# Optimization experiments

Hardware: AMD Instinct MI355X
Metric: run time of the kernel (lower is better)

Reference implementation:

```python
import jax, jax.numpy as jnp
import numpy as np

N_PTS = 500_000
NP_NODES = 258
L_DOMAIN = 10.0
TP = 1.0 - 1.0 / 150.0  # threshold_p
TM = 1.0 + 1.0 / 150.0  # threshold_m


def setup_inputs() -> dict:
    key = jax.random.key(0)
    k_x, _ = jax.random.split(key)
    x = jax.random.uniform(k_x, (N_PTS, 1), dtype=jnp.float32) * L_DOMAIN
    coordinates = jnp.linspace(0.0, L_DOMAIN, NP_NODES, dtype=jnp.float32)
    w_uu = jnp.ones((NP_NODES - 2,), dtype=jnp.float32)   # NodalValues_uu init
    w_dd = jnp.zeros((2,), dtype=jnp.float32)             # [u_0, u_L] = [0, 0]
    return {"x": x, "coordinates": coordinates, "w_uu": w_uu, "w_dd": w_dd}


def _hat(x, xm, xi, xp):
    # Piecewise-linear 'hat' basis: LinearBlock(left) + LinearBlock(right) + l2 bias (-1)
    left = jax.nn.relu(jax.nn.relu(xi - x) * (-1.0 / (xi - xm)) + 1.0)
    right = jax.nn.relu(jax.nn.relu(x - xi) * (-1.0 / (xp - xi)) + 1.0)
    return left + right - 1.0


def reference(x, coordinates, w_uu, w_dd):
    c = coordinates
    # Interior nodes i = 1 .. np-2 (vectorized over all shape functions)
    xm = c[:-2]          # x_{i-1}, shape [np-2]
    xi = c[1:-1]         # x_i
    xp = c[2:]           # x_{i+1}
    xi = jnp.maximum(jnp.minimum(xi, TP * xp), TM * xm)
    phi_uu = _hat(x, xm, xi, xp)          # [N, np-2] via broadcast of x [N,1]

    # Boundary shape functions (Shapefunction(-1) and Shapefunction(-2))
    xm0 = c[0] - c[-1] / 100.0
    xi0 = jnp.maximum(jnp.minimum(c[0], TP * c[1]), TM * xm0)
    xpL = c[-1] * (1.0 + 1.0 / 100.0)
    xiL = jnp.maximum(jnp.minimum(c[-1], TP * xpL), TM * c[-2])
    phi_0 = _hat(x, xm0, xi0, c[1])       # [N, 1]
    phi_L = _hat(x, c[-2], xiL, xpL)      # [N, 1]
    phi_dd = jnp.concatenate([phi_0, phi_L], axis=1)  # [N, 2]

    # InterpoLayer_uu + InterpoLayer_dd + SumLayer (weights all ones -> sum)
    u = phi_uu @ w_uu + phi_dd @ w_dd     # [N]
    return u[:, None]                     # [N, 1]
```

## Files before the change

kernel.cpp:

```cpp
#include <hip/hip_runtime.h>


#define TPf ((float)(1.0 - 1.0 / 150.0))
#define TMf ((float)(1.0 + 1.0 / 150.0))

__device__ __forceinline__ float hat_eval(float x, float xm, float xi, float xp) {
    float l = fmaxf(fmaxf(xi - x, 0.0f) * (-1.0f / (xi - xm)) + 1.0f, 0.0f);
    float r = fmaxf(fmaxf(x - xi, 0.0f) * (-1.0f / (xp - xi)) + 1.0f, 0.0f);
    return l + r - 1.0f;
}

__global__ __launch_bounds__(256) void MeshNN_29042568855825_kernel(
    const float* __restrict__ X,
    const float* __restrict__ C,
    const float* __restrict__ Wu,
    const float* __restrict__ Wd,
    float* __restrict__ Out,
    int n)
{
    __shared__ float sc[258];
    __shared__ float sw[256];
    __shared__ float swd[2];
    const int tid = threadIdx.x;
    for (int j = tid; j < 258; j += 256) sc[j] = C[j];
    sw[tid] = Wu[tid];
    if (tid < 2) swd[tid] = Wd[tid];
    __syncthreads();

    const float c0 = sc[0], c1 = sc[1], cNm2 = sc[256], cNm1 = sc[257];
    const float xm0 = c0 - cNm1 / 100.0f;
    const float xi0 = fmaxf(fminf(c0, TPf * c1), TMf * xm0);
    const float xpL = cNm1 * (float)(1.0 + 1.0 / 100.0);
    const float xiL = fmaxf(fminf(cNm1, TPf * xpL), TMf * cNm2);
    const float inv_h = 257.0f / (cNm1 - c0);
    const float wd0 = swd[0], wd1 = swd[1];

    const int g = blockIdx.x * 256 + tid;
    const int base = g * 4;
    if (base >= n) return;

    float xs[4];
    const bool full = (base + 3) < n;
    if (full) {
        float4 xv = ((const float4*)X)[g];
        xs[0] = xv.x; xs[1] = xv.y; xs[2] = xv.z; xs[3] = xv.w;
    } else {
        #pragma unroll
        for (int k = 0; k < 4; ++k) xs[k] = (base + k < n) ? X[base + k] : 0.0f;
    }

    float us[4];
    #pragma unroll
    for (int k = 0; k < 4; ++k) {
        const float x = xs[k];
        int i = (int)((x - c0) * inv_h);
        i = min(max(i, 0), 256);
        while (i > 0 && x < sc[i]) --i;
        while (i < 256 && x >= sc[i + 1]) ++i;

        float u = wd0 * hat_eval(x, xm0, xi0, c1)
                + wd1 * hat_eval(x, cNm2, xiL, xpL);

        if (i >= 1) {
            const float xm = sc[i - 1], xr = sc[i], xp = sc[i + 1];
            const float xic = fmaxf(fminf(xr, TPf * xp), TMf * xm);
            u += sw[i - 1] * hat_eval(x, xm, xic, xp);
        }
        if (i <= 255) {
            const float xm = sc[i], xr = sc[i + 1], xp = sc[i + 2];
            const float xic = fmaxf(fminf(xr, TPf * xp), TMf * xm);
            u += sw[i] * hat_eval(x, xm, xic, xp);
        }
        us[k] = u;
    }

    if (full) {
        ((float4*)Out)[g] = make_float4(us[0], us[1], us[2], us[3]);
    } else {
        #pragma unroll
        for (int k = 0; k < 4; ++k)
            if (base + k < n) Out[base + k] = us[k];
    }
}

extern "C" void kernel_launch(void* const* d_in, const int* in_sizes, int n_in,
                              void* d_out, int out_size, void* d_ws, size_t ws_size,
                              hipStream_t stream) {
    const float* x  = (const float*)d_in[0];
    const float* c  = (const float*)d_in[1];
    const float* wu = (const float*)d_in[2];
    const float* wd = (const float*)d_in[3];
    float* out = (float*)d_out;

    const int n = in_sizes[0];
    const int ngroups = (n + 3) / 4;
    const int blocks = (ngroups + 255) / 256;
    MeshNN_29042568855825_kernel<<<blocks, 256, 0, stream>>>(x, c, wu, wd, out, n);
}
```

Measured before the change: 63.49 us.

## Precompute per-element hat parameters in shared memory, one point per thread

Each block now precomputes the clamped node positions and the left/right reciprocal widths of every interior shape function, plus the boundary function parameters, in shared memory. This removes the per-point divisions. The kernel also drops the float4 four-points-per-thread layout and processes one point per thread, which launches four times as many blocks. Every block now pays a larger prologue with extra divisions and a second barrier, so the setup cost is amortised over fewer points.

```diff
diff --git a/kernel.cpp b/kernel.cpp
--- a/kernel.cpp
+++ b/kernel.cpp
@@ -4,9 +4,10 @@
 #define TPf ((float)(1.0 - 1.0 / 150.0))
 #define TMf ((float)(1.0 + 1.0 / 150.0))
 
-__device__ __forceinline__ float hat_eval(float x, float xm, float xi, float xp) {
-    float l = fmaxf(fmaxf(xi - x, 0.0f) * (-1.0f / (xi - xm)) + 1.0f, 0.0f);
-    float r = fmaxf(fmaxf(x - xi, 0.0f) * (-1.0f / (xp - xi)) + 1.0f, 0.0f);
+__device__ __forceinline__ float hat_rcp(float x, float xm, float xi, float xp,
+                                         float rl, float rr) {
+    float l = fmaxf(fmaxf(xi - x, 0.0f) * (-rl) + 1.0f, 0.0f);
+    float r = fmaxf(fmaxf(x - xi, 0.0f) * (-rr) + 1.0f, 0.0f);
     return l + r - 1.0f;
 }
 
@@ -19,68 +20,64 @@
     int n)
 {
     __shared__ float sc[258];
+    __shared__ float sxi[256];
+    __shared__ float srl[256];
+    __shared__ float srr[256];
     __shared__ float sw[256];
-    __shared__ float swd[2];
+    __shared__ float sb[12];
+
     const int tid = threadIdx.x;
     for (int j = tid; j < 258; j += 256) sc[j] = C[j];
-    sw[tid] = Wu[tid];
-    if (tid < 2) swd[tid] = Wd[tid];
     __syncthreads();
 
-    const float c0 = sc[0], c1 = sc[1], cNm2 = sc[256], cNm1 = sc[257];
-    const float xm0 = c0 - cNm1 / 100.0f;
-    const float xi0 = fmaxf(fminf(c0, TPf * c1), TMf * xm0);
-    const float xpL = cNm1 * (float)(1.0 + 1.0 / 100.0);
-    const float xiL = fmaxf(fminf(cNm1, TPf * xpL), TMf * cNm2);
-    const float inv_h = 257.0f / (cNm1 - c0);
-    const float wd0 = swd[0], wd1 = swd[1];
+    {
+        const int j = tid;
+        const float xm = sc[j], xr = sc[j + 1], xp = sc[j + 2];
+        const float xic = fmaxf(fminf(xr, TPf * xp), TMf * xm);
+        sxi[j] = xic;
+        srl[j] = 1.0f / (xic - xm);
+        srr[j] = 1.0f / (xp - xic);
+        sw[j]  = Wu[j];
+    }
+    if (tid == 0) {
+        const float c0 = sc[0], c1 = sc[1], cNm2 = sc[256], cNm1 = sc[257];
+        const float xm0 = c0 - cNm1 / 100.0f;
+        const float xi0 = fmaxf(fminf(c0, TPf * c1), TMf * xm0);
+        const float xpL = cNm1 * (float)(1.0 + 1.0 / 100.0);
+        const float xiL = fmaxf(fminf(cNm1, TPf * xpL), TMf * cNm2);
+        sb[0] = xm0;  sb[1] = xi0;  sb[2] = c1;
+        sb[3] = 1.0f / (xi0 - xm0); sb[4] = 1.0f / (c1 - xi0);
+        sb[5] = cNm2; sb[6] = xiL;  sb[7] = xpL;
+        sb[8] = 1.0f / (xiL - cNm2); sb[9] = 1.0f / (xpL - xiL);
+        sb[10] = Wd[0]; sb[11] = Wd[1];
+    }
+    __syncthreads();
 
-    const int g = blockIdx.x * 256 + tid;
-    const int base = g * 4;
-    if (base >= n) return;
+    const int idx = blockIdx.x * 256 + tid;
+    if (idx >= n) return;
 
-    float xs[4];
-    const bool full = (base + 3) < n;
-    if (full) {
-        float4 xv = ((const float4*)X)[g];
-        xs[0] = xv.x; xs[1] = xv.y; xs[2] = xv.z; xs[3] = xv.w;
-    } else {
-        #pragma unroll
-        for (int k = 0; k < 4; ++k) xs[k] = (base + k < n) ? X[base + k] : 0.0f;
+    const float c0 = sc[0];
+    const float inv_h = 257.0f / (sc[257] - c0);
+    const float x = X[idx];
+
+    int i = (int)((x - c0) * inv_h);
+    i = min(max(i, 0), 256);
+    while (i > 0 && x < sc[i]) --i;
+    while (i < 256 && x >= sc[i + 1]) ++i;
+
+    float u = sb[10] * hat_rcp(x, sb[0], sb[1], sb[2], sb[3], sb[4])
+            + sb[11] * hat_rcp(x, sb[5], sb[6], sb[7], sb[8], sb[9]);
+
+    if (i >= 1) {
+        const int j = i - 1;
+        u += sw[j] * hat_rcp(x, sc[j], sxi[j], sc[j + 2], srl[j], srr[j]);
+    }
+    if (i <= 255) {
+        const int j = i;
+        u += sw[j] * hat_rcp(x, sc[j], sxi[j], sc[j + 2], srl[j], srr[j]);
     }
 
-    float us[4];
-    #pragma unroll
-    for (int k = 0; k < 4; ++k) {
-        const float x = xs[k];
-        int i = (int)((x - c0) * inv_h);
-        i = min(max(i, 0), 256);
-        while (i > 0 && x < sc[i]) --i;
-        while (i < 256 && x >= sc[i + 1]) ++i;
-
-        float u = wd0 * hat_eval(x, xm0, xi0, c1)
-                + wd1 * hat_eval(x, cNm2, xiL, xpL);
-
-        if (i >= 1) {
-            const float xm = sc[i - 1], xr = sc[i], xp = sc[i + 1];
-            const float xic = fmaxf(fminf(xr, TPf * xp), TMf * xm);
-            u += sw[i - 1] * hat_eval(x, xm, xic, xp);
-        }
-        if (i <= 255) {
-            const float xm = sc[i], xr = sc[i + 1], xp = sc[i + 2];
-            const float xic = fmaxf(fminf(xr, TPf * xp), TMf * xm);
-            u += sw[i] * hat_eval(x, xm, xic, xp);
-        }
-        us[k] = u;
-    }
-
-    if (full) {
-        ((float4*)Out)[g] = make_float4(us[0], us[1], us[2], us[3]);
-    } else {
-        #pragma unroll
-        for (int k = 0; k < 4; ++k)
-            if (base + k < n) Out[base + k] = us[k];
-    }
+    Out[idx] = u;
 }
 
 extern "C" void kernel_launch(void* const* d_in, const int* in_sizes, int n_in,
@@ -93,7 +90,6 @@
     float* out = (float*)d_out;
 
     const int n = in_sizes[0];
-    const int ngroups = (n + 3) / 4;
-    const int blocks = (ngroups + 255) / 256;
+    const int blocks = (n + 255) / 256;
     MeshNN_29042568855825_kernel<<<blocks, 256, 0, stream>>>(x, c, wu, wd, out, n);
 }
```

Measured after the change: 62.26 us. Within noise of the previous version (-1.9%).
